# Kernel optimization log

Hardware: AMD Instinct MI355X
Metric: run time of the kernel (lower is better)

The kernel has to match this reference:

```python
import jax, jax.numpy as jnp
import numpy as np

B, C, N, K = 2, 64, 20000, 16
COUT = 64


def setup_inputs() -> dict:
    key = jax.random.key(0)
    k1, k2, k3, k4, k5 = jax.random.split(key, 5)
    x = jax.random.normal(k1, (B, C, N, 1), dtype=jnp.float32)
    edge_index = jax.random.randint(k2, (2, B, N, K), 0, N)
    pos = jax.random.normal(k3, (B, 3, N, 1), dtype=jnp.float32)
    # BasicConv([2C, COUT]) -> 1x1 Conv2d weight [COUT, 2C] (+bias), then ReLU
    W = jax.random.normal(k4, (COUT, 2 * C), dtype=jnp.float32) * (1.0 / np.sqrt(2 * C))
    b = jax.random.normal(k5, (COUT,), dtype=jnp.float32) * 0.01
    return {"x": x, "edge_index": edge_index, "pos": pos, "W": W, "b": b}


def _gather(t, idx):
    # t: [B, C, N, 1], idx: [B, N, K] -> [B, C, N, K]
    t3 = t[..., 0]  # [B, C, N]
    return jax.vmap(lambda tb, ib: tb[:, ib])(t3, idx)


def reference(x, edge_index, pos, W, b):
    x_i = _gather(x, edge_index[1])           # [B, C, N, K] center
    x_j = _gather(x, edge_index[0])           # [B, C, N, K] neighbor
    feat = jnp.concatenate([x_i, x_j - x_i], axis=1)  # [B, 2C, N, K]
    # 1x1 conv + bias + ReLU
    out = jnp.einsum('oc,bcnk->bonk', W, feat) + b[None, :, None, None]
    out = jax.nn.relu(out)
    # distance-based suppression
    pos_i = _gather(pos, edge_index[1])       # [B, 3, N, K]
    pos_j = _gather(pos, edge_index[0])
    dis = jnp.sqrt(jnp.sum(jnp.square(pos_j - pos_i), axis=1))  # [B, N, K]
    suppression = 2.0 * jax.nn.sigmoid(-dis)[:, None, :, :]     # [B, 1, N, K]
    out = out * suppression
    max_value = jnp.max(out, axis=-1, keepdims=True)             # [B, COUT, N, 1]
    return max_value
```

## Files before the change

### kernel.cpp

```cpp
#include <hip/hip_runtime.h>
#include <math.h>

#define B_    2
#define C_    64
#define N_    20000
#define K_    16
#define COUT_ 64
#define TN1   64
#define NB1   ((N_ + TN1 - 1) / TN1)
#define TN2   32
#define NB2   (N_ / TN2)

typedef unsigned int   u32;
typedef unsigned short u16;

static __device__ __forceinline__ u16 f2bf(float f) {
    union { float f; u32 u; } v; v.f = f;
    u32 r = (v.u + 0x7FFFu + ((v.u >> 16) & 1u)) >> 16;
    return (u16)r;
}
static __device__ __forceinline__ float uasf(u32 u) {
    union { u32 u; float f; } v; v.u = u; return v.f;
}

__global__ __launch_bounds__(256)
void stage1(const float* __restrict__ x, const int* __restrict__ ei,
            const float* __restrict__ pos, const float* __restrict__ W,
            const float* __restrict__ bias,
            u16* __restrict__ zbuf, u16* __restrict__ ybuf,
            uint2* __restrict__ es) {
    __shared__ float xt[64][68];
    __shared__ float wc[64][130];

    const int bi   = blockIdx.x;
    const int b    = bi / NB1;
    const int n0   = (bi % NB1) * TN1;
    const int t    = threadIdx.x;
    const int lane = t & 63;
    const int w    = t >> 6;

    #pragma unroll
    for (int r = 0; r < 16; ++r) {
        int flat = r * 256 + t;
        int o = flat >> 6, c = flat & 63;
        float w1 = W[o * 128 + c];
        float w2 = W[o * 128 + 64 + c];
        wc[c][2 * o]     = w1 - w2;
        wc[c][2 * o + 1] = w2;
    }
    const float* xb = x + (size_t)b * C_ * N_;
    #pragma unroll
    for (int r = 0; r < 4; ++r) {
        int flat = r * 256 + t;
        int c = flat >> 4, ng = (flat & 15) * 4;
        int n = n0 + ng;
        float4 v;
        if (n + 3 < N_) {
            v = *(const float4*)&xb[c * N_ + n];
        } else {
            v.x = (n     < N_) ? xb[c * N_ + n    ] : 0.0f;
            v.y = (n + 1 < N_) ? xb[c * N_ + n + 1] : 0.0f;
            v.z = (n + 2 < N_) ? xb[c * N_ + n + 2] : 0.0f;
            v.w = (n + 3 < N_) ? xb[c * N_ + n + 3] : 0.0f;
        }
        *(float4*)&xt[c][ng] = v;
    }
    const float bo = bias[lane];
    __syncthreads();

    const int nb = w * 16;
    float4 z0 = {bo,bo,bo,bo}, z1 = z0, z2 = z0, z3 = z0;
    float4 y0 = {0,0,0,0},     y1 = y0, y2 = y0, y3 = y0;

#define FMA4(ZR, YR, XV) \
    ZR.x = fmaf(wv.x, XV.x, ZR.x);  YR.x = fmaf(wv.y, XV.x, YR.x); \
    ZR.y = fmaf(wv.x, XV.y, ZR.y);  YR.y = fmaf(wv.y, XV.y, YR.y); \
    ZR.z = fmaf(wv.x, XV.z, ZR.z);  YR.z = fmaf(wv.y, XV.z, YR.z); \
    ZR.w = fmaf(wv.x, XV.w, ZR.w);  YR.w = fmaf(wv.y, XV.w, YR.w);

    #pragma unroll 2
    for (int c = 0; c < 64; ++c) {
        float2 wv = *(const float2*)&wc[c][2 * lane];
        float4 xa = *(const float4*)&xt[c][nb];
        float4 xv1 = *(const float4*)&xt[c][nb + 4];
        float4 xv2 = *(const float4*)&xt[c][nb + 8];
        float4 xv3 = *(const float4*)&xt[c][nb + 12];
        FMA4(z0, y0, xa)
        FMA4(z1, y1, xv1)
        FMA4(z2, y2, xv2)
        FMA4(z3, y3, xv3)
    }
#undef FMA4

    {
        const size_t rowb = (size_t)b * N_;
        auto st = [&](int i, float zv, float yv) {
            int n = n0 + nb + i;
            if (n < N_) {
                size_t off = (rowb + n) * 64 + lane;
                zbuf[off] = f2bf(zv);
                ybuf[off] = f2bf(yv);
            }
        };
        st(0,  z0.x, y0.x); st(1,  z0.y, y0.y); st(2,  z0.z, y0.z); st(3,  z0.w, y0.w);
        st(4,  z1.x, y1.x); st(5,  z1.y, y1.y); st(6,  z1.z, y1.z); st(7,  z1.w, y1.w);
        st(8,  z2.x, y2.x); st(9,  z2.y, y2.y); st(10, z2.z, y2.z); st(11, z2.w, y2.w);
        st(12, z3.x, y3.x); st(13, z3.y, y3.y); st(14, z3.z, y3.z); st(15, z3.w, y3.w);
    }

    const int*   e0 = ei + (size_t)b * N_ * K_;
    const int*   e1 = ei + ((size_t)B_ + b) * N_ * K_;
    const float* pb = pos + (size_t)b * 3 * N_;
    uint2* esb = es + (size_t)b * N_ * K_;
    #pragma unroll
    for (int i = 0; i < 4; ++i) {
        int idx = n0 * K_ + i * 256 + t;
        if (idx < N_ * K_) {
            int i0 = e0[idx], i1 = e1[idx];
            float dx = pb[i0]          - pb[i1];
            float dy = pb[N_ + i0]     - pb[N_ + i1];
            float dz = pb[2 * N_ + i0] - pb[2 * N_ + i1];
            float dis = sqrtf(dx * dx + dy * dy + dz * dz);
            float s = 2.0f / (1.0f + __expf(dis));
            esb[idx] = make_uint2((u32)i0 | ((u32)i1 << 16), __float_as_uint(s));
        }
    }
}

__global__ __launch_bounds__(256)
void stage2(const uint2* __restrict__ es,
            const u16* __restrict__ zbuf, const u16* __restrict__ ybuf,
            float* __restrict__ out) {
    __shared__ uint2 esl[TN2][17];
    __shared__ float tile[TN2][66];

    const int bi   = blockIdx.x;
    const int b    = bi / NB2;
    const int n0   = (bi % NB2) * TN2;
    const int t    = threadIdx.x;
    const int lane = t & 63;
    const int w    = t >> 6;
    const int n8   = lane >> 3;
    const int cq   = lane & 7;

    const uint2* esb = es + (size_t)b * N_ * K_ + (size_t)n0 * K_;
    #pragma unroll
    for (int r = 0; r < 2; ++r) {
        int idx = r * 256 + t;
        esl[idx >> 4][idx & 15] = esb[idx];
    }
    __syncthreads();

    const u16* zb = zbuf + (size_t)b * N_ * 64;
    const u16* yb = ybuf + (size_t)b * N_ * 64;
    const int  nl = w * 8 + n8;

    float4 ma = {0,0,0,0}, mb = {0,0,0,0};

#define COMB(ZW, YW, MLO, MHI) { \
    float zl = uasf((ZW) << 16), zh = uasf((ZW) & 0xFFFF0000u); \
    float yl = uasf((YW) << 16), yh = uasf((YW) & 0xFFFF0000u); \
    MLO = fmaxf(MLO, fmaxf(zl + yl, 0.0f) * s); \
    MHI = fmaxf(MHI, fmaxf(zh + yh, 0.0f) * s); }

    #pragma unroll 4
    for (int k = 0; k < K_; ++k) {
        uint2 e = esl[nl][k];
        int   i0 = (int)(e.x & 0xFFFFu);
        int   i1 = (int)(e.x >> 16);
        float s  = uasf(e.y);
        uint4 z4 = *((const uint4*)(zb + ((size_t)i1 << 6)) + cq);
        uint4 y4 = *((const uint4*)(yb + ((size_t)i0 << 6)) + cq);
        COMB(z4.x, y4.x, ma.x, ma.y)
        COMB(z4.y, y4.y, ma.z, ma.w)
        COMB(z4.z, y4.z, mb.x, mb.y)
        COMB(z4.w, y4.w, mb.z, mb.w)
    }
#undef COMB

    {
        int cb = cq * 8;
        *(float2*)&tile[nl][cb]     = make_float2(ma.x, ma.y);
        *(float2*)&tile[nl][cb + 2] = make_float2(ma.z, ma.w);
        *(float2*)&tile[nl][cb + 4] = make_float2(mb.x, mb.y);
        *(float2*)&tile[nl][cb + 6] = make_float2(mb.z, mb.w);
    }
    __syncthreads();

    #pragma unroll
    for (int r = 0; r < 8; ++r) {
        int flat = r * 256 + t;
        int o = flat >> 5, n2 = flat & 31;
        out[((size_t)b * COUT_ + o) * N_ + n0 + n2] = tile[n2][o];
    }
}

extern "C" void kernel_launch(void* const* d_in, const int* in_sizes, int n_in,
                              void* d_out, int out_size, void* d_ws, size_t ws_size,
                              hipStream_t stream) {
    const float* x    = (const float*)d_in[0];
    const int*   ei   = (const int*)  d_in[1];
    const float* pos  = (const float*)d_in[2];
    const float* W    = (const float*)d_in[3];
    const float* bias = (const float*)d_in[4];
    float*       out  = (float*)d_out;

    const size_t tabElems = (size_t)B_ * N_ * 64;
    u16*   zbuf = (u16*)d_ws;
    u16*   ybuf = zbuf + tabElems;
    uint2* es   = (uint2*)(ybuf + tabElems);

    hipLaunchKernelGGL(stage1, dim3(B_ * NB1), dim3(256), 0, stream,
                       x, ei, pos, W, bias, zbuf, ybuf, es);
    hipLaunchKernelGGL(stage2, dim3(B_ * NB2), dim3(256), 0, stream,
                       es, zbuf, ybuf, out);
}
```

Baseline: 112.7 us.

## Parallelize stage2 over neighbors with wave-shuffle max reduction

Restructures the gather/max kernel so that each wavefront handles one point, with its 16 neighbors spread across lanes. Every lane loads 32 channels of the z and y rows at once, and the max over K is then taken with xor shuffles. This removes the serial K loop and the shared-memory staging of edge data, so more independent gather loads are in flight at the same time. In exchange it adds shuffle work, uses 1024-thread blocks that cover fewer points, and leaves many lanes idle during the final store.

Measured after the change: 127.3 us. 13.0% more time.

```diff
diff --git a/kernel.cpp b/kernel.cpp
--- a/kernel.cpp
+++ b/kernel.cpp
@@ -8,7 +8,7 @@
 #define COUT_ 64
 #define TN1   64
 #define NB1   ((N_ + TN1 - 1) / TN1)
-#define TN2   32
+#define TN2   16
 #define NB2   (N_ / TN2)
 
 typedef unsigned int   u32;
@@ -127,70 +127,74 @@
     }
 }
 
-__global__ __launch_bounds__(256)
+__global__ __launch_bounds__(1024)
 void stage2(const uint2* __restrict__ es,
             const u16* __restrict__ zbuf, const u16* __restrict__ ybuf,
             float* __restrict__ out) {
-    __shared__ uint2 esl[TN2][17];
-    __shared__ float tile[TN2][66];
+    __shared__ float tile[TN2][68];
 
     const int bi   = blockIdx.x;
     const int b    = bi / NB2;
     const int n0   = (bi % NB2) * TN2;
     const int t    = threadIdx.x;
+    const int w    = t >> 6;
     const int lane = t & 63;
-    const int w    = t >> 6;
-    const int n8   = lane >> 3;
-    const int cq   = lane & 7;
-
-    const uint2* esb = es + (size_t)b * N_ * K_ + (size_t)n0 * K_;
-    #pragma unroll
-    for (int r = 0; r < 2; ++r) {
-        int idx = r * 256 + t;
-        esl[idx >> 4][idx & 15] = esb[idx];
-    }
-    __syncthreads();
-
-    const u16* zb = zbuf + (size_t)b * N_ * 64;
-    const u16* yb = ybuf + (size_t)b * N_ * 64;
-    const int  nl = w * 8 + n8;
-
-    float4 ma = {0,0,0,0}, mb = {0,0,0,0};
-
-#define COMB(ZW, YW, MLO, MHI) { \
+    const int k    = lane >> 2;
+    const int c2   = lane & 3;
+
+    const int n = n0 + w;
+    uint2 e = es[(size_t)b * N_ * K_ + (size_t)n * K_ + k];
+    const int   i0 = (int)(e.x & 0xFFFFu);
+    const int   i1 = (int)(e.x >> 16);
+    const float s  = uasf(e.y);
+
+    const u16* zr = zbuf + (size_t)b * N_ * 64 + ((size_t)i1 << 6) + c2 * 16;
+    const u16* yr = ybuf + (size_t)b * N_ * 64 + ((size_t)i0 << 6) + c2 * 16;
+    uint4 z4a = *(const uint4*)zr;
+    uint4 z4b = *(const uint4*)(zr + 8);
+    uint4 y4a = *(const uint4*)yr;
+    uint4 y4b = *(const uint4*)(yr + 8);
+
+#define MKV(ZW, YW, VLO, VHI) { \
     float zl = uasf((ZW) << 16), zh = uasf((ZW) & 0xFFFF0000u); \
     float yl = uasf((YW) << 16), yh = uasf((YW) & 0xFFFF0000u); \
-    MLO = fmaxf(MLO, fmaxf(zl + yl, 0.0f) * s); \
-    MHI = fmaxf(MHI, fmaxf(zh + yh, 0.0f) * s); }
-
-    #pragma unroll 4
-    for (int k = 0; k < K_; ++k) {
-        uint2 e = esl[nl][k];
-        int   i0 = (int)(e.x & 0xFFFFu);
-        int   i1 = (int)(e.x >> 16);
-        float s  = uasf(e.y);
-        uint4 z4 = *((const uint4*)(zb + ((size_t)i1 << 6)) + cq);
-        uint4 y4 = *((const uint4*)(yb + ((size_t)i0 << 6)) + cq);
-        COMB(z4.x, y4.x, ma.x, ma.y)
-        COMB(z4.y, y4.y, ma.z, ma.w)
-        COMB(z4.z, y4.z, mb.x, mb.y)
-        COMB(z4.w, y4.w, mb.z, mb.w)
-    }
-#undef COMB
+    VLO = fmaxf(zl + yl, 0.0f) * s; \
+    VHI = fmaxf(zh + yh, 0.0f) * s; }
+
+    float4 va, vb, vc, vd;
+    MKV(z4a.x, y4a.x, va.x, va.y)
+    MKV(z4a.y, y4a.y, va.z, va.w)
+    MKV(z4a.z, y4a.z, vb.x, vb.y)
+    MKV(z4a.w, y4a.w, vb.z, vb.w)
+    MKV(z4b.x, y4b.x, vc.x, vc.y)
+    MKV(z4b.y, y4b.y, vc.z, vc.w)
+    MKV(z4b.z, y4b.z, vd.x, vd.y)
+    MKV(z4b.w, y4b.w, vd.z, vd.w)
+#undef MKV
+
+#define R4(V, ST) \
+    V.x = fmaxf(V.x, __shfl_xor(V.x, ST)); \
+    V.y = fmaxf(V.y, __shfl_xor(V.y, ST)); \
+    V.z = fmaxf(V.z, __shfl_xor(V.z, ST)); \
+    V.w = fmaxf(V.w, __shfl_xor(V.w, ST));
+    R4(va, 4)  R4(vb, 4)  R4(vc, 4)  R4(vd, 4)
+    R4(va, 8)  R4(vb, 8)  R4(vc, 8)  R4(vd, 8)
+    R4(va, 16) R4(vb, 16) R4(vc, 16) R4(vd, 16)
+    R4(va, 32) R4(vb, 32) R4(vc, 32) R4(vd, 32)
+#undef R4
+
+    if (k == 0) {
+        int cb = c2 * 16;
+        *(float4*)&tile[w][cb]      = va;
+        *(float4*)&tile[w][cb + 4]  = vb;
+        *(float4*)&tile[w][cb + 8]  = vc;
+        *(float4*)&tile[w][cb + 12] = vd;
+    }
+    __syncthreads();
 
     {
-        int cb = cq * 8;
-        *(float2*)&tile[nl][cb]     = make_float2(ma.x, ma.y);
-        *(float2*)&tile[nl][cb + 2] = make_float2(ma.z, ma.w);
-        *(float2*)&tile[nl][cb + 4] = make_float2(mb.x, mb.y);
-        *(float2*)&tile[nl][cb + 6] = make_float2(mb.z, mb.w);
-    }
-    __syncthreads();
-
-    #pragma unroll
-    for (int r = 0; r < 8; ++r) {
-        int flat = r * 256 + t;
-        int o = flat >> 5, n2 = flat & 31;
+        int o  = t >> 4;
+        int n2 = t & 15;
         out[((size_t)b * COUT_ + o) * N_ + n0 + n2] = tile[n2][o];
     }
 }
@@ -212,6 +216,6 @@
 
     hipLaunchKernelGGL(stage1, dim3(B_ * NB1), dim3(256), 0, stream,
                        x, ei, pos, W, bias, zbuf, ybuf, es);
-    hipLaunchKernelGGL(stage2, dim3(B_ * NB2), dim3(256), 0, stream,
+    hipLaunchKernelGGL(stage2, dim3(B_ * NB2), dim3(1024), 0, stream,
                        es, zbuf, ybuf, out);
 }
```
